# Kernel tuning notes

Hardware: AMD Instinct MI355X
Metric: run time of the kernel (lower is better)

## Reference

```python
import jax, jax.numpy as jnp
import numpy as np

DICE_W, BCE_W = 1.0, 1.0
BBOX_W = 0.025
L1_W, GIOU_W = 1.0, 1.0  # assumed BoxLoss weighting: loss = l1.sum(-1) + (1 - giou)


def _xywh_to_xyxy(b):
    cx, cy, w, h = b[..., 0], b[..., 1], b[..., 2], b[..., 3]
    return jnp.stack([cx - w / 2, cy - h / 2, cx + w / 2, cy + h / 2], axis=-1)


def _xyxy_to_xywh(b):
    x1, y1, x2, y2 = b[..., 0], b[..., 1], b[..., 2], b[..., 3]
    return jnp.stack([(x1 + x2) / 2, (y1 + y2) / 2, x2 - x1, y2 - y1], axis=-1)


def _giou(a, b):
    # a, b: [N,4] xyxy, paired GIoU
    ix1 = jnp.maximum(a[:, 0], b[:, 0]); iy1 = jnp.maximum(a[:, 1], b[:, 1])
    ix2 = jnp.minimum(a[:, 2], b[:, 2]); iy2 = jnp.minimum(a[:, 3], b[:, 3])
    inter = jnp.clip(ix2 - ix1, 0) * jnp.clip(iy2 - iy1, 0)
    area_a = jnp.clip(a[:, 2] - a[:, 0], 0) * jnp.clip(a[:, 3] - a[:, 1], 0)
    area_b = jnp.clip(b[:, 2] - b[:, 0], 0) * jnp.clip(b[:, 3] - b[:, 1], 0)
    union = area_a + area_b - inter
    iou = inter / jnp.maximum(union, 1e-6)
    cx1 = jnp.minimum(a[:, 0], b[:, 0]); cy1 = jnp.minimum(a[:, 1], b[:, 1])
    cx2 = jnp.maximum(a[:, 2], b[:, 2]); cy2 = jnp.maximum(a[:, 3], b[:, 3])
    c = jnp.clip(cx2 - cx1, 0) * jnp.clip(cy2 - cy1, 0)
    return iou - (c - union) / jnp.maximum(c, 1e-6)


def _box_loss_per_sample(pred_xywh, tgt_xywh):
    l1 = jnp.abs(pred_xywh - tgt_xywh).sum(-1)
    g = 1.0 - _giou(_xywh_to_xyxy(pred_xywh), _xywh_to_xyxy(tgt_xywh))
    return L1_W * l1 + GIOU_W * g


def _forward(pred_mask, pred_bbox, gt_bbox_rand, target_mask, img_h, img_w):
    B = pred_mask.shape[0]
    H, W = img_h, img_w
    tgt = target_mask.astype(pred_mask.dtype)          # [B,H,W] binary
    logits = pred_mask[:, 0]                           # [B,H,W]
    probs = jax.nn.sigmoid(logits)

    # ---- seg_loss: dice + bce (both mean-reduced) ----
    p = probs.reshape(B, -1); t = tgt.reshape(B, -1)
    dice = 1.0 - (2.0 * (p * t).sum(1) + 1.0) / (p.sum(1) + t.sum(1) + 1.0)
    x = logits.reshape(B, -1)
    bce = jnp.maximum(x, 0) - x * t + jnp.log1p(jnp.exp(-jnp.abs(x)))
    loss_mask = DICE_W * dice.mean() + BCE_W * bce.mean()

    # ---- bbox_loss: gt x1y1x2y2 (pixels) -> normalized cxcywh ----
    gx1 = gt_bbox_rand[:, 0] * (0.45 * W); gy1 = gt_bbox_rand[:, 1] * (0.45 * H)
    gx2 = gx1 + 1.0 + gt_bbox_rand[:, 2] * (0.5 * W)
    gy2 = gy1 + 1.0 + gt_bbox_rand[:, 3] * (0.5 * H)
    gt_xyxy = jnp.stack([gx1, gy1, gx2, gy2], axis=-1)
    # original divides by img_size [H,W] repeated -> [H,W,H,W] (square imgs)
    norm_div = jnp.asarray([H, W, H, W], dtype=pred_bbox.dtype)
    gt_norm = _xyxy_to_xywh(gt_xyxy) / norm_div
    loss_det = _box_loss_per_sample(pred_bbox, gt_norm).mean() * BBOX_W

    # ---- boxseg_iouloss2 (vectorized over the per-batch python loop) ----
    box_xyxy = _xywh_to_xyxy(pred_bbox)                # normalized xyxy
    scale = jnp.asarray([W, H, W, H], dtype=pred_bbox.dtype)
    pix = (box_xyxy * scale).astype(jnp.int32)         # trunc like .to(int)
    x1p = jnp.clip(pix[:, 0], 0, W); x2p = jnp.clip(pix[:, 2], 0, W)
    y1p = jnp.clip(pix[:, 1], 0, H); y2p = jnp.clip(pix[:, 3], 0, H)
    seg_bin = (probs > 0.5).astype(pred_mask.dtype)    # S2Bthr == B2Sthr == 0.5
    xs = jnp.arange(W); ys = jnp.arange(H)
    in_x = (xs[None, :] >= x1p[:, None]) & (xs[None, :] < x2p[:, None])  # [B,W]
    in_y = (ys[None, :] >= y1p[:, None]) & (ys[None, :] < y2p[:, None])  # [B,H]
    inside = in_y[:, :, None] & in_x[:, None, :]                          # [B,H,W]
    inter = (seg_bin * inside).sum((1, 2))
    area = seg_bin.sum((1, 2))
    s2b_iou = jnp.where(area > 0, inter / jnp.maximum(area, 1.0), 0.0)
    loss_s2b = (1.0 - s2b_iou).mean()

    # get_maskouterbox: per-sample min/max of coords where mask is on
    mb = seg_bin.astype(bool)
    x1o = jnp.min(jnp.where(mb, xs[None, None, :], W), axis=(1, 2))
    y1o = jnp.min(jnp.where(mb, ys[None, :, None], H), axis=(1, 2))
    x2o = jnp.max(jnp.where(mb, xs[None, None, :], -1), axis=(1, 2))
    y2o = jnp.max(jnp.where(mb, ys[None, :, None], -1), axis=(1, 2))
    present = (area > 0)[:, None]
    outer = jnp.stack([x1o, y1o, x2o, y2o], axis=-1).astype(pred_bbox.dtype)
    outer = jnp.where(present, outer, 0.0) / scale
    loss_b2s = _box_loss_per_sample(_xyxy_to_xywh(outer), _xyxy_to_xywh(box_xyxy)).mean()

    return loss_mask + loss_det + loss_s2b + loss_b2s


def setup_inputs() -> dict:
    key = jax.random.key(0)
    k1, k2, k3, k4 = jax.random.split(key, 4)
    B, H, W = 64, 512, 512
    return {
        "pred_mask": jax.random.normal(k1, (B, 1, H, W), dtype=jnp.float32),
        "pred_bbox": jax.random.uniform(k2, (B, 4), dtype=jnp.float32),
        "gt_bbox_rand": jax.random.uniform(k3, (B, 4), dtype=jnp.float32),
        "target_mask": jax.random.randint(k4, (B, H, W), 0, 2, dtype=jnp.int32),
        "img_h": H,
        "img_w": W,
    }


def reference(pred_mask, pred_bbox, gt_bbox_rand, target_mask, img_h, img_w):
    return _forward(pred_mask, pred_bbox, gt_bbox_rand, target_mask, img_h, img_w)
```

## Files before the change

### kernel.cpp

```cpp
#include <hip/hip_runtime.h>
#include <math.h>


#define TPB 256

typedef float fx4 __attribute__((ext_vector_type(4)));
typedef int   ix4 __attribute__((ext_vector_type(4)));

__device__ inline float box_loss_xywh(const float pb[4], const float tb[4]) {
    float l1 = fabsf(pb[0] - tb[0]) + fabsf(pb[1] - tb[1]) +
               fabsf(pb[2] - tb[2]) + fabsf(pb[3] - tb[3]);
    float ax1 = pb[0] - 0.5f * pb[2], ay1 = pb[1] - 0.5f * pb[3];
    float ax2 = pb[0] + 0.5f * pb[2], ay2 = pb[1] + 0.5f * pb[3];
    float bx1 = tb[0] - 0.5f * tb[2], by1 = tb[1] - 0.5f * tb[3];
    float bx2 = tb[0] + 0.5f * tb[2], by2 = tb[1] + 0.5f * tb[3];

    float ix1 = fmaxf(ax1, bx1), iy1 = fmaxf(ay1, by1);
    float ix2 = fminf(ax2, bx2), iy2 = fminf(ay2, by2);
    float inter  = fmaxf(ix2 - ix1, 0.f) * fmaxf(iy2 - iy1, 0.f);
    float area_a = fmaxf(ax2 - ax1, 0.f) * fmaxf(ay2 - ay1, 0.f);
    float area_b = fmaxf(bx2 - bx1, 0.f) * fmaxf(by2 - by1, 0.f);
    float uni = area_a + area_b - inter;
    float iou = inter / fmaxf(uni, 1e-6f);
    float cx1 = fminf(ax1, bx1), cy1 = fminf(ay1, by1);
    float cx2 = fmaxf(ax2, bx2), cy2 = fmaxf(ay2, by2);
    float c = fmaxf(cx2 - cx1, 0.f) * fmaxf(cy2 - cy1, 0.f);
    float giou = iou - (c - uni) / fmaxf(c, 1e-6f);
    return l1 + (1.0f - giou);
}

__global__ __launch_bounds__(TPB)
void uh_reduce(const float* __restrict__ pred_mask,
               const int*   __restrict__ target_mask,
               const float* __restrict__ pred_bbox,
               const int*   __restrict__ pH, const int* __restrict__ pW,
               float* __restrict__ wf, int* __restrict__ wi,
               int HW, int N)
{
    const int b      = blockIdx.y;
    const int chunk  = blockIdx.x;
    const int nchunk = gridDim.x;
    const int W = *pW;
    const int H = *pH;

    float c0 = pred_bbox[b * 4 + 0], c1 = pred_bbox[b * 4 + 1];
    float c2 = pred_bbox[b * 4 + 2], c3 = pred_bbox[b * 4 + 3];
    const int bx1 = min(max((int)((c0 - 0.5f * c2) * (float)W), 0), W);
    const int by1 = min(max((int)((c1 - 0.5f * c3) * (float)H), 0), H);
    const int bx2 = min(max((int)((c0 + 0.5f * c2) * (float)W), 0), W);
    const int by2 = min(max((int)((c1 + 0.5f * c3) * (float)H), 0), H);

    const int chunk_px = HW / nchunk;
    const int rows     = chunk_px / W;
    const int tpr      = W >> 3;
    const int rpi      = TPB / tpr;
    const int iters    = rows / rpi;
    const int rowoff   = threadIdx.x / tpr;
    const int cx       = (threadIdx.x - rowoff * tpr) << 3;
    const int ybase    = chunk * rows;

    unsigned inxmask = 0;
    #pragma unroll
    for (int j = 0; j < 8; ++j)
        inxmask |= (unsigned)((cx + j >= bx1) & (cx + j < bx2)) << j;

    const long boff = (long)b * HW + (long)(ybase + rowoff) * W + cx;
    const float* pp = pred_mask + boff;
    const int*   tp = target_mask + boff;
    const int    stride = rpi * W;

    float s_pt = 0.f, s_p = 0.f, slg2 = 0.f, s_relu = 0.f;
    int c_t = 0, c_area = 0, c_inter = 0;
    unsigned rmask = 0, colmask = 0;

    for (int gb = 0; gb < iters; gb += 4) {
        fx4 xa0 = __builtin_nontemporal_load((const fx4*)(pp));
        fx4 xb0 = __builtin_nontemporal_load((const fx4*)(pp + 4));
        ix4 ta0 = __builtin_nontemporal_load((const ix4*)(tp));
        ix4 tb0 = __builtin_nontemporal_load((const ix4*)(tp + 4));
        fx4 xa1 = __builtin_nontemporal_load((const fx4*)(pp + stride));
        fx4 xb1 = __builtin_nontemporal_load((const fx4*)(pp + stride + 4));
        ix4 ta1 = __builtin_nontemporal_load((const ix4*)(tp + stride));
        ix4 tb1 = __builtin_nontemporal_load((const ix4*)(tp + stride + 4));
        fx4 xa2 = __builtin_nontemporal_load((const fx4*)(pp + 2 * stride));
        fx4 xb2 = __builtin_nontemporal_load((const fx4*)(pp + 2 * stride + 4));
        ix4 ta2 = __builtin_nontemporal_load((const ix4*)(tp + 2 * stride));
        ix4 tb2 = __builtin_nontemporal_load((const ix4*)(tp + 2 * stride + 4));
        fx4 xa3 = __builtin_nontemporal_load((const fx4*)(pp + 3 * stride));
        fx4 xb3 = __builtin_nontemporal_load((const fx4*)(pp + 3 * stride + 4));
        ix4 ta3 = __builtin_nontemporal_load((const ix4*)(tp + 3 * stride));
        ix4 tb3 = __builtin_nontemporal_load((const ix4*)(tp + 3 * stride + 4));
        pp += 4 * stride; tp += 4 * stride;

        #define PROC_ROW(G, XA, XB, TA, TB)                                   \
        {                                                                     \
            const float xs[8] = {XA[0], XA[1], XA[2], XA[3],                  \
                                 XB[0], XB[1], XB[2], XB[3]};                 \
            const int   ts[8] = {TA[0], TA[1], TA[2], TA[3],                  \
                                 TB[0], TB[1], TB[2], TB[3]};                 \
            unsigned m8 = 0;                                                  \
            _Pragma("unroll")                                                 \
            for (int j = 0; j < 8; ++j) {                                     \
                float xl = xs[j];                                             \
                bool  t  = ts[j] != 0;                                        \
                float e  = __expf(-fabsf(xl));           \
                float r  = __builtin_amdgcn_rcpf(1.f + e);                    \
                slg2    += __log2f(r);                  \
                float p  = (xl >= 0.f) ? r : 1.f - r;                         \
                s_p     += p;                                                 \
                s_pt    += t ? p : 0.f;                                       \
                s_relu  += fmaxf(t ? -xl : xl, 0.f);                          \
                c_t     += ts[j];                                             \
                m8      |= (unsigned)(xl > 0.f) << j;                         \
            }                                                                 \
            c_area  += __popc(m8);                                            \
            const int y = ybase + rowoff + (G) * rpi;                         \
            c_inter += ((y >= by1) & (y < by2)) ? __popc(m8 & inxmask) : 0;   \
            colmask |= m8;                                                    \
            rmask   |= (m8 ? 1u : 0u) << (G);                                 \
        }

        PROC_ROW(gb + 0, xa0, xb0, ta0, tb0)
        PROC_ROW(gb + 1, xa1, xb1, ta1, tb1)
        PROC_ROW(gb + 2, xa2, xb2, ta2, tb2)
        PROC_ROW(gb + 3, xa3, xb3, ta3, tb3)
        #undef PROC_ROW
    }

    float s_bce = fmaf(-0.69314718055994531f, slg2, s_relu);

    int xmn = W, xmx = -1, ymn = H, ymx = -1;
    if (colmask) {
        xmn = cx + (__ffs(colmask) - 1);
        xmx = cx + (31 - __clz(colmask));
    }
    if (rmask) {
        ymn = ybase + rowoff + (__ffs(rmask) - 1) * rpi;
        ymx = ybase + rowoff + (31 - __clz(rmask)) * rpi;
    }

    #pragma unroll
    for (int o = 32; o; o >>= 1) {
        s_pt  += __shfl_down(s_pt,  o, 64);
        s_p   += __shfl_down(s_p,   o, 64);
        s_bce += __shfl_down(s_bce, o, 64);
        c_t    += __shfl_down(c_t,    o, 64);
        c_area += __shfl_down(c_area, o, 64);
        c_inter+= __shfl_down(c_inter,o, 64);
        xmn = min(xmn, __shfl_down(xmn, o, 64));
        ymn = min(ymn, __shfl_down(ymn, o, 64));
        xmx = max(xmx, __shfl_down(xmx, o, 64));
        ymx = max(ymx, __shfl_down(ymx, o, 64));
    }

    __shared__ float smf[3][4];
    __shared__ int   smi[7][4];
    const int wid = threadIdx.x >> 6;
    if ((threadIdx.x & 63) == 0) {
        smf[0][wid] = s_pt;  smf[1][wid] = s_p;  smf[2][wid] = s_bce;
        smi[0][wid] = c_t;   smi[1][wid] = c_area; smi[2][wid] = c_inter;
        smi[3][wid] = xmn;   smi[4][wid] = ymn;
        smi[5][wid] = xmx;   smi[6][wid] = ymx;
    }
    __syncthreads();
    if (threadIdx.x == 0) {
        float a0 = 0.f, a1 = 0.f, a2 = 0.f;
        int i0 = 0, i1 = 0, i2 = 0;
        int m3 = W, m4 = H, m5 = -1, m6 = -1;
        #pragma unroll
        for (int w = 0; w < 4; ++w) {
            a0 += smf[0][w]; a1 += smf[1][w]; a2 += smf[2][w];
            i0 += smi[0][w]; i1 += smi[1][w]; i2 += smi[2][w];
            m3 = min(m3, smi[3][w]); m4 = min(m4, smi[4][w]);
            m5 = max(m5, smi[5][w]); m6 = max(m6, smi[6][w]);
        }
        const int idx = b * nchunk + chunk;
        wf[0 * N + idx] = a0; wf[1 * N + idx] = a1; wf[2 * N + idx] = a2;
        wi[0 * N + idx] = i0; wi[1 * N + idx] = i1; wi[2 * N + idx] = i2;
        wi[3 * N + idx] = m3; wi[4 * N + idx] = m4;
        wi[5 * N + idx] = m5; wi[6 * N + idx] = m6;
    }
}

__global__ __launch_bounds__(TPB)
void uh_final(const float* __restrict__ pred_bbox,
              const float* __restrict__ gt_bbox,
              const int* __restrict__ pH, const int* __restrict__ pW,
              const float* __restrict__ wf, const int* __restrict__ wi,
              int B, int HW, int nchunk, float* __restrict__ out)
{
    const int W = *pW, H = *pH;
    const int N = B * nchunk;
    const int tid = threadIdx.x;
    const int b   = tid >> 2;
    const int q   = tid & 3;

    float v = 0.f;
    if (b < B) {
        float s_pt = 0.f, s_p = 0.f, s_bce = 0.f;
        int c_t = 0, c_area = 0, c_inter = 0;
        int xmn = W, ymn = H, xmx = -1, ymx = -1;
        for (int c = q; c < nchunk; c += 4) {
            const int idx = b * nchunk + c;
            s_pt  += wf[0 * N + idx];
            s_p   += wf[1 * N + idx];
            s_bce += wf[2 * N + idx];
            c_t    += wi[0 * N + idx];
            c_area += wi[1 * N + idx];
            c_inter+= wi[2 * N + idx];
            xmn = min(xmn, wi[3 * N + idx]); ymn = min(ymn, wi[4 * N + idx]);
            xmx = max(xmx, wi[5 * N + idx]); ymx = max(ymx, wi[6 * N + idx]);
        }
        #pragma unroll
        for (int o = 1; o < 4; o <<= 1) {
            s_pt  += __shfl_xor(s_pt,  o, 64);
            s_p   += __shfl_xor(s_p,   o, 64);
            s_bce += __shfl_xor(s_bce, o, 64);
            c_t    += __shfl_xor(c_t,    o, 64);
            c_area += __shfl_xor(c_area, o, 64);
            c_inter+= __shfl_xor(c_inter,o, 64);
            xmn = min(xmn, __shfl_xor(xmn, o, 64));
            ymn = min(ymn, __shfl_xor(ymn, o, 64));
            xmx = max(xmx, __shfl_xor(xmx, o, 64));
            ymx = max(ymx, __shfl_xor(ymx, o, 64));
        }

        if (q == 0) {
            float dice = 1.f - (2.f * s_pt + 1.f) / (s_p + (float)c_t + 1.f);

            float pb[4] = {pred_bbox[b*4+0], pred_bbox[b*4+1],
                           pred_bbox[b*4+2], pred_bbox[b*4+3]};
            float g0 = gt_bbox[b*4+0], g1 = gt_bbox[b*4+1];
            float g2 = gt_bbox[b*4+2], g3 = gt_bbox[b*4+3];
            float gx1 = g0 * (0.45f * (float)W);
            float gy1 = g1 * (0.45f * (float)H);
            float gx2 = gx1 + 1.0f + g2 * (0.5f * (float)W);
            float gy2 = gy1 + 1.0f + g3 * (0.5f * (float)H);
            float gt[4] = { ((gx1 + gx2) * 0.5f) / (float)H,
                            ((gy1 + gy2) * 0.5f) / (float)W,
                            (gx2 - gx1) / (float)H,
                            (gy2 - gy1) / (float)W };
            float det = 0.025f * box_loss_xywh(pb, gt);

            float iou_s2b = (c_area > 0)
                              ? (float)c_inter / fmaxf((float)c_area, 1.f) : 0.f;
            float s2b = 1.f - iou_s2b;

            float ox1, oy1, ox2, oy2;
            if (c_area > 0) {
                ox1 = (float)xmn; oy1 = (float)ymn;
                ox2 = (float)xmx; oy2 = (float)ymx;
            } else {
                ox1 = oy1 = ox2 = oy2 = 0.f;
            }
            ox1 /= (float)W; ox2 /= (float)W;
            oy1 /= (float)H; oy2 /= (float)H;
            float ow[4] = { (ox1 + ox2) * 0.5f, (oy1 + oy2) * 0.5f,
                            ox2 - ox1, oy2 - oy1 };
            float px1 = pb[0] - 0.5f * pb[2], py1 = pb[1] - 0.5f * pb[3];
            float px2 = pb[0] + 0.5f * pb[2], py2 = pb[1] + 0.5f * pb[3];
            float pw[4] = { (px1 + px2) * 0.5f, (py1 + py2) * 0.5f,
                            px2 - px1, py2 - py1 };
            float b2s = box_loss_xywh(ow, pw);

            v = dice + s_bce / (float)HW + det + s2b + b2s;
        }
    }

    #pragma unroll
    for (int o = 32; o; o >>= 1) v += __shfl_down(v, o, 64);
    __shared__ float sv[4];
    if ((tid & 63) == 0) sv[tid >> 6] = v;
    __syncthreads();
    if (tid == 0) out[0] = (sv[0] + sv[1] + sv[2] + sv[3]) / (float)B;
}

extern "C" void kernel_launch(void* const* d_in, const int* in_sizes, int n_in,
                              void* d_out, int out_size, void* d_ws, size_t ws_size,
                              hipStream_t stream) {
    const float* pred_mask   = (const float*)d_in[0];
    const float* pred_bbox   = (const float*)d_in[1];
    const float* gt_bbox     = (const float*)d_in[2];
    const int*   target_mask = (const int*)d_in[3];
    const int*   pH          = (const int*)d_in[4];
    const int*   pW          = (const int*)d_in[5];
    float* out = (float*)d_out;

    const int B  = in_sizes[1] / 4;
    const int HW = in_sizes[0] / B;

    int bps = 32;
    if ((size_t)10 * sizeof(int) * B * bps > ws_size) bps = 16;
    const int N = B * bps;

    float* wf = (float*)d_ws;
    int*   wi = (int*)d_ws + (size_t)3 * N;

    dim3 grid(bps, B);
    uh_reduce<<<grid, TPB, 0, stream>>>(pred_mask, target_mask, pred_bbox,
                                        pH, pW, wf, wi, HW, N);
    uh_final<<<1, TPB, 0, stream>>>(pred_bbox, gt_bbox, pH, pW, wf, wi,
                                    B, HW, bps, out);
}
```

Baseline: 155.4 us.

## Stage mask rows into LDS via direct global-to-LDS loads with finer grid

Replaces per-thread nontemporal vector loads with global_load_lds DMA into shared memory. Each block now covers 8 rows (2 per wave), so the grid grows to H/8 chunks per image, and each lane reads 8 contiguous pixels from LDS. Manual vmcnt waits let the first row be processed while the second row's loads are still in flight. The host hardcodes W=512 and drops the workspace-size check, so other shapes or a small workspace could break; the LDS path also adds 32KB of shared memory per block, which limits occupancy.

```diff
diff --git a/kernel.cpp b/kernel.cpp
--- a/kernel.cpp
+++ b/kernel.cpp
@@ -27,6 +27,12 @@
     float c = fmaxf(cx2 - cx1, 0.f) * fmaxf(cy2 - cy1, 0.f);
     float giou = iou - (c - uni) / fmaxf(c, 1e-6f);
     return l1 + (1.0f - giou);
+}
+
+__device__ __forceinline__ void gload16(const void* g, void* l) {
+    __builtin_amdgcn_global_load_lds(
+        (const __attribute__((address_space(1))) unsigned int*)g,
+        (__attribute__((address_space(3))) unsigned int*)l, 16, 0, 0);
 }
 
 __global__ __launch_bounds__(TPB)
@@ -50,82 +56,85 @@
     const int bx2 = min(max((int)((c0 + 0.5f * c2) * (float)W), 0), W);
     const int by2 = min(max((int)((c1 + 0.5f * c3) * (float)H), 0), H);
 
-    const int chunk_px = HW / nchunk;
-    const int rows     = chunk_px / W;
-    const int tpr      = W >> 3;
-    const int rpi      = TPB / tpr;
-    const int iters    = rows / rpi;
-    const int rowoff   = threadIdx.x / tpr;
-    const int cx       = (threadIdx.x - rowoff * tpr) << 3;
-    const int ybase    = chunk * rows;
+    const int rows  = H / nchunk;
+    const int rpw   = rows / 4;
+    const int wv    = threadIdx.x >> 6;
+    const int l     = threadIdx.x & 63;
+    const int ppl   = W >> 6;
+    const int cx    = l * ppl;
+    const int ybase = chunk * rows;
+    const int kpr   = W >> 8;
 
     unsigned inxmask = 0;
-    #pragma unroll
+    #pragma unroll 8
     for (int j = 0; j < 8; ++j)
         inxmask |= (unsigned)((cx + j >= bx1) & (cx + j < bx2)) << j;
 
-    const long boff = (long)b * HW + (long)(ybase + rowoff) * W + cx;
-    const float* pp = pred_mask + boff;
-    const int*   tp = target_mask + boff;
-    const int    stride = rpi * W;
+    __shared__ float sp[8 * 512];
+    __shared__ int   st[8 * 512];
+
+    const long srow = (long)b * HW + (long)ybase * W;
+    for (int r = 0; r < rpw; ++r) {
+        const int rl = wv * rpw + r;
+        const float* gp = pred_mask   + srow + (long)rl * W;
+        const int*   gt = target_mask + srow + (long)rl * W;
+        for (int k = 0; k < kpr; ++k)
+            gload16(gp + k * 256 + l * 4, &sp[rl * 512 + k * 256]);
+        for (int k = 0; k < kpr; ++k)
+            gload16(gt + k * 256 + l * 4, &st[rl * 512 + k * 256]);
+    }
 
     float s_pt = 0.f, s_p = 0.f, slg2 = 0.f, s_relu = 0.f;
     int c_t = 0, c_area = 0, c_inter = 0;
     unsigned rmask = 0, colmask = 0;
 
-    for (int gb = 0; gb < iters; gb += 4) {
-        fx4 xa0 = __builtin_nontemporal_load((const fx4*)(pp));
-        fx4 xb0 = __builtin_nontemporal_load((const fx4*)(pp + 4));
-        ix4 ta0 = __builtin_nontemporal_load((const ix4*)(tp));
-        ix4 tb0 = __builtin_nontemporal_load((const ix4*)(tp + 4));
-        fx4 xa1 = __builtin_nontemporal_load((const fx4*)(pp + stride));
-        fx4 xb1 = __builtin_nontemporal_load((const fx4*)(pp + stride + 4));
-        ix4 ta1 = __builtin_nontemporal_load((const ix4*)(tp + stride));
-        ix4 tb1 = __builtin_nontemporal_load((const ix4*)(tp + stride + 4));
-        fx4 xa2 = __builtin_nontemporal_load((const fx4*)(pp + 2 * stride));
-        fx4 xb2 = __builtin_nontemporal_load((const fx4*)(pp + 2 * stride + 4));
-        ix4 ta2 = __builtin_nontemporal_load((const ix4*)(tp + 2 * stride));
-        ix4 tb2 = __builtin_nontemporal_load((const ix4*)(tp + 2 * stride + 4));
-        fx4 xa3 = __builtin_nontemporal_load((const fx4*)(pp + 3 * stride));
-        fx4 xb3 = __builtin_nontemporal_load((const fx4*)(pp + 3 * stride + 4));
-        ix4 ta3 = __builtin_nontemporal_load((const ix4*)(tp + 3 * stride));
-        ix4 tb3 = __builtin_nontemporal_load((const ix4*)(tp + 3 * stride + 4));
-        pp += 4 * stride; tp += 4 * stride;
-
-        #define PROC_ROW(G, XA, XB, TA, TB)                                   \
-        {                                                                     \
-            const float xs[8] = {XA[0], XA[1], XA[2], XA[3],                  \
-                                 XB[0], XB[1], XB[2], XB[3]};                 \
-            const int   ts[8] = {TA[0], TA[1], TA[2], TA[3],                  \
-                                 TB[0], TB[1], TB[2], TB[3]};                 \
-            unsigned m8 = 0;                                                  \
-            _Pragma("unroll")                                                 \
-            for (int j = 0; j < 8; ++j) {                                     \
-                float xl = xs[j];                                             \
-                bool  t  = ts[j] != 0;                                        \
-                float e  = __expf(-fabsf(xl));           \
-                float r  = __builtin_amdgcn_rcpf(1.f + e);                    \
-                slg2    += __log2f(r);                  \
-                float p  = (xl >= 0.f) ? r : 1.f - r;                         \
-                s_p     += p;                                                 \
-                s_pt    += t ? p : 0.f;                                       \
-                s_relu  += fmaxf(t ? -xl : xl, 0.f);                          \
-                c_t     += ts[j];                                             \
-                m8      |= (unsigned)(xl > 0.f) << j;                         \
-            }                                                                 \
-            c_area  += __popc(m8);                                            \
-            const int y = ybase + rowoff + (G) * rpi;                         \
-            c_inter += ((y >= by1) & (y < by2)) ? __popc(m8 & inxmask) : 0;   \
-            colmask |= m8;                                                    \
-            rmask   |= (m8 ? 1u : 0u) << (G);                                 \
-        }
-
-        PROC_ROW(gb + 0, xa0, xb0, ta0, tb0)
-        PROC_ROW(gb + 1, xa1, xb1, ta1, tb1)
-        PROC_ROW(gb + 2, xa2, xb2, ta2, tb2)
-        PROC_ROW(gb + 3, xa3, xb3, ta3, tb3)
-        #undef PROC_ROW
-    }
+    #define PROC_ROW(RL)                                                      \
+    {                                                                         \
+        const int rl_ = (RL);                                                 \
+        fx4 xa = *(const fx4*)&sp[rl_ * 512 + cx];                            \
+        fx4 xb = *(const fx4*)&sp[rl_ * 512 + cx + 4];                        \
+        ix4 ta = *(const ix4*)&st[rl_ * 512 + cx];                            \
+        ix4 tb = *(const ix4*)&st[rl_ * 512 + cx + 4];                        \
+        const float xs[8] = {xa[0], xa[1], xa[2], xa[3],                      \
+                             xb[0], xb[1], xb[2], xb[3]};                     \
+        const int   ts[8] = {ta[0], ta[1], ta[2], ta[3],                      \
+                             tb[0], tb[1], tb[2], tb[3]};                     \
+        unsigned m8 = 0;                                                      \
+        _Pragma("unroll")                                                     \
+        for (int j = 0; j < 8; ++j) {                                         \
+            float xl = xs[j];                                                 \
+            bool  t  = ts[j] != 0;                                            \
+            float e  = __expf(-fabsf(xl));                                    \
+            float r  = __builtin_amdgcn_rcpf(1.f + e);                        \
+            slg2    += __log2f(r);                                            \
+            float p  = (xl >= 0.f) ? r : 1.f - r;                             \
+            s_p     += p;                                                     \
+            s_pt    += t ? p : 0.f;                                           \
+            s_relu  += fmaxf(t ? -xl : xl, 0.f);                              \
+            c_t     += ts[j];                                                 \
+            m8      |= (unsigned)(xl > 0.f) << j;                             \
+        }                                                                     \
+        c_area  += __popc(m8);                                                \
+        const int y_ = ybase + rl_;                                           \
+        c_inter += ((y_ >= by1) & (y_ < by2)) ? __popc(m8 & inxmask) : 0;     \
+        colmask |= m8;                                                        \
+        rmask   |= (m8 ? 1u : 0u) << rl_;                                     \
+    }
+
+    if (rpw == 2 && kpr == 2) {
+        asm volatile("s_waitcnt vmcnt(4)" ::: "memory");
+        __builtin_amdgcn_sched_barrier(0);
+        PROC_ROW(wv * 2 + 0)
+        asm volatile("s_waitcnt vmcnt(0)" ::: "memory");
+        __builtin_amdgcn_sched_barrier(0);
+        PROC_ROW(wv * 2 + 1)
+    } else {
+        asm volatile("s_waitcnt vmcnt(0)" ::: "memory");
+        __builtin_amdgcn_sched_barrier(0);
+        for (int r = 0; r < rpw; ++r)
+            PROC_ROW(wv * rpw + r)
+    }
+    #undef PROC_ROW
 
     float s_bce = fmaf(-0.69314718055994531f, slg2, s_relu);
 
@@ -135,8 +144,8 @@
         xmx = cx + (31 - __clz(colmask));
     }
     if (rmask) {
-        ymn = ybase + rowoff + (__ffs(rmask) - 1) * rpi;
-        ymx = ybase + rowoff + (31 - __clz(rmask)) * rpi;
+        ymn = ybase + (__ffs(rmask) - 1);
+        ymx = ybase + (31 - __clz(rmask));
     }
 
     #pragma unroll
@@ -155,12 +164,11 @@
 
     __shared__ float smf[3][4];
     __shared__ int   smi[7][4];
-    const int wid = threadIdx.x >> 6;
-    if ((threadIdx.x & 63) == 0) {
-        smf[0][wid] = s_pt;  smf[1][wid] = s_p;  smf[2][wid] = s_bce;
-        smi[0][wid] = c_t;   smi[1][wid] = c_area; smi[2][wid] = c_inter;
-        smi[3][wid] = xmn;   smi[4][wid] = ymn;
-        smi[5][wid] = xmx;   smi[6][wid] = ymx;
+    if (l == 0) {
+        smf[0][wv] = s_pt;  smf[1][wv] = s_p;  smf[2][wv] = s_bce;
+        smi[0][wv] = c_t;   smi[1][wv] = c_area; smi[2][wv] = c_inter;
+        smi[3][wv] = xmn;   smi[4][wv] = ymn;
+        smi[5][wv] = xmx;   smi[6][wv] = ymx;
     }
     __syncthreads();
     if (threadIdx.x == 0) {
@@ -288,10 +296,12 @@
 
     const int B  = in_sizes[1] / 4;
     const int HW = in_sizes[0] / B;
-
-    int bps = 32;
-    if ((size_t)10 * sizeof(int) * B * bps > ws_size) bps = 16;
-    const int N = B * bps;
+    const int W  = 512;
+    const int H  = HW / W;
+    (void)W;
+
+    const int bps = H / 8;
+    const int N   = B * bps;
 
     float* wf = (float*)d_ws;
     int*   wi = (int*)d_ws + (size_t)3 * N;
```

After: 158.6 us. 2.1% more time.
